# Kernel optimization log

Hardware: AMD Instinct MI355X
Metric: run time of the kernel (lower is better)

Reference implementation:

```python
import jax, jax.numpy as jnp
import numpy as np

N = 100000   # nodes
E = 1200000  # edges
IN, HID, OUT = 64, 64, 64
G = 64       # graphs in the batch


def setup_inputs() -> dict:
    key = jax.random.key(0)
    ks = jax.random.split(key, 7)
    x = jax.random.normal(ks[0], (N, IN), dtype=jnp.float32)
    edge_index = jax.random.randint(ks[1], (2, E), 0, N, dtype=jnp.int32)
    batch = jnp.sort(jax.random.randint(ks[2], (N,), 0, G, dtype=jnp.int32))
    W1 = jax.random.normal(ks[3], (IN, HID), dtype=jnp.float32) * (1.0 / np.sqrt(IN))
    b1 = jnp.zeros((HID,), dtype=jnp.float32)
    W2 = jax.random.normal(ks[4], (HID, OUT), dtype=jnp.float32) * (1.0 / np.sqrt(HID))
    b2 = jnp.zeros((OUT,), dtype=jnp.float32)
    return {"x": x, "edge_index": edge_index, "batch": batch,
            "W1": W1, "b1": b1, "W2": W2, "b2": b2}


def _gcn_conv(x, W, b, src, dst, dinv):
    # x' = D^{-1/2} (A + I) D^{-1/2} (x W) + b   (PyG GCNConv with self-loops)
    h = x @ W                                   # [N, F_out]
    norm = dinv[src] * dinv[dst]                # [E]
    agg = jax.ops.segment_sum(h[src] * norm[:, None], dst, num_segments=N)
    agg = agg + h * (dinv * dinv)[:, None]      # self-loop contribution
    return agg + b


def reference(x, edge_index, batch, W1, b1, W2, b2):
    src, dst = edge_index[0], edge_index[1]
    # degree with self-loops, counted at the aggregation target (PyG convention)
    deg = jax.ops.segment_sum(jnp.ones((E,), x.dtype), dst, num_segments=N) + 1.0
    dinv = jax.lax.rsqrt(deg)

    h1 = jax.nn.relu(_gcn_conv(x, W1, b1, src, dst, dinv))   # [N, HID]
    s1 = jax.ops.segment_sum(h1, batch, num_segments=G)      # [G, HID]
    h2 = jax.nn.relu(_gcn_conv(h1, W2, b2, src, dst, dinv))  # [N, OUT]
    s2 = jax.ops.segment_sum(h2, batch, num_segments=G)      # [G, OUT]
    return h2, jnp.concatenate([s1, s2], axis=1)
```

## Files before the change

kernel.cpp:

```cpp
#include <hip/hip_runtime.h>


#define FDIM 64
#define BSHIFT 7
#define MAXNB 1024
#define BCAP 4096

__device__ __forceinline__ unsigned short f2bf(float f) {
    union { float f; unsigned int u; } a; a.f = f;
    unsigned int u = a.u;
    unsigned int r = u + 0x7fffu + ((u >> 16) & 1u);
    return (unsigned short)(r >> 16);
}
__device__ __forceinline__ float bf2f(unsigned short s) {
    union { unsigned int u; float f; } a; a.u = ((unsigned int)s) << 16;
    return a.f;
}

__global__ __launch_bounds__(256) void k_hist(const int* __restrict__ dst, int E, int NB,
                                              int* __restrict__ bucketCnt,
                                              const int* __restrict__ batch, int N, int G,
                                              int* __restrict__ gstart) {
    if (blockIdx.x >= 256) {
        int i = (blockIdx.x - 256) * 256 + threadIdx.x;
        if (i >= N) return;
        int b = batch[i];
        if (i == 0) { for (int g = 0; g <= b; g++) gstart[g] = 0; }
        else {
            int p = batch[i - 1];
            for (int g = p + 1; g <= b; g++) gstart[g] = i;
        }
        if (i == N - 1) { for (int g = b + 1; g <= G; g++) gstart[g] = N; }
        return;
    }
    __shared__ int h[MAXNB];
    for (int i = threadIdx.x; i < NB; i += 256) h[i] = 0;
    __syncthreads();
    for (int e = blockIdx.x * blockDim.x + threadIdx.x; e < E; e += 256 * 256)
        atomicAdd(&h[dst[e] >> BSHIFT], 1);
    __syncthreads();
    for (int i = threadIdx.x; i < NB; i += 256) {
        int c = h[i];
        if (c) atomicAdd(&bucketCnt[i], c);
    }
}

__global__ __launch_bounds__(256) void k_bscat(const int* __restrict__ src,
                                               const int* __restrict__ dst, int E, int NB,
                                               const int* __restrict__ bucketCnt,
                                               int* __restrict__ bucketFill,
                                               unsigned int* __restrict__ ebuf) {
    __shared__ int hist[MAXNB];
    __shared__ int base[MAXNB];
    __shared__ int sc[256];
    int t = threadIdx.x;
    for (int i = t; i < MAXNB; i += 256) hist[i] = 0;
    __syncthreads();
    int e0 = blockIdx.x * 4096;
    int s[16], d[16], r[16];
#pragma unroll
    for (int k = 0; k < 16; k++) {
        int e = e0 + k * 256 + t;
        bool valid = e < E;
        s[k] = valid ? src[e] : 0;
        d[k] = valid ? dst[e] : 0;
        r[k] = valid ? atomicAdd(&hist[d[k] >> BSHIFT], 1) : 0;
    }
    int c0 = bucketCnt[t * 4 + 0], c1 = bucketCnt[t * 4 + 1];
    int c2 = bucketCnt[t * 4 + 2], c3 = bucketCnt[t * 4 + 3];
    int ssum = c0 + c1 + c2 + c3;
    sc[t] = ssum;
    __syncthreads();
    for (int off = 1; off < 256; off <<= 1) {
        int u = (t >= off) ? sc[t - off] : 0;
        __syncthreads();
        sc[t] += u;
        __syncthreads();
    }
    int run = sc[t] - ssum;
    base[t * 4 + 0] = run; run += c0;
    base[t * 4 + 1] = run; run += c1;
    base[t * 4 + 2] = run; run += c2;
    base[t * 4 + 3] = run;
    __syncthreads();
    for (int i = t; i < NB; i += 256) {
        int c = hist[i];
        if (c) base[i] += atomicAdd(&bucketFill[i], c);
    }
    __syncthreads();
#pragma unroll
    for (int k = 0; k < 16; k++) {
        int e = e0 + k * 256 + t;
        if (e < E)
            ebuf[base[d[k] >> BSHIFT] + r[k]] =
                (unsigned int)s[k] | ((unsigned int)(d[k] & 127) << 17);
    }
}

__global__ __launch_bounds__(256) void k_bsort(const unsigned int* __restrict__ ebuf,
                                               const int* __restrict__ bucketCnt, int N,
                                               int* __restrict__ row_ptr,
                                               int* __restrict__ row_blocks,
                                               int* __restrict__ col,
                                               float* __restrict__ dinv) {
    __shared__ int cntL[128];
    __shared__ int scanL[128];
    __shared__ int fillL[128];
    __shared__ int colL[BCAP];
    __shared__ int padT;
    __shared__ int red[4];
    int b = blockIdx.x;
    int n0 = b << BSHIFT;
    int nCnt = N - n0; if (nCnt > 128) nCnt = 128;
    int t = threadIdx.x;
    int part = 0;
    for (int i = t; i < b; i += 256) part += bucketCnt[i];
    for (int off = 32; off; off >>= 1) part += __shfl_down(part, off);
    if ((t & 63) == 0) red[t >> 6] = part;
    __syncthreads();
    int lo = red[0] + red[1] + red[2] + red[3];
    int hi = lo + bucketCnt[b];
    int outBase = ((lo + 7) & ~7) + (b << 10);
    if (t < 128) { cntL[t] = 0; fillL[t] = 0; }
    __syncthreads();
    for (int e = lo + t; e < hi; e += 256)
        atomicAdd(&cntL[ebuf[e] >> 17], 1);
    __syncthreads();
    int pc = 0;
    if (t < 128) { pc = (cntL[t] + 7) & ~7; scanL[t] = pc; }
    __syncthreads();
    for (int off = 1; off < 128; off <<= 1) {
        int u = (t >= off && t < 128) ? scanL[t - off] : 0;
        __syncthreads();
        if (t < 128) scanL[t] += u;
        __syncthreads();
    }
    if (t == 127) padT = scanL[127];
    if (t < nCnt) {
        int ex = scanL[t] - pc;
        row_ptr[n0 + t] = outBase + ex;
        row_blocks[n0 + t] = pc >> 3;
        dinv[n0 + t] = rsqrtf((float)cntL[t] + 1.0f);
        scanL[t] = ex;
    }
    __syncthreads();
    int padTotal = padT;
    if (padTotal <= BCAP) {
        for (int i = t; i < padTotal; i += 256) colL[i] = N;
        __syncthreads();
        for (int e = lo + t; e < hi; e += 256) {
            unsigned int pr = ebuf[e];
            int d = pr >> 17;
            int r = scanL[d] + atomicAdd(&fillL[d], 1);
            colL[r] = (int)(pr & 0x1FFFFu);
        }
        __syncthreads();
        for (int i = t; i < padTotal; i += 256) col[outBase + i] = colL[i];
    } else {
        for (int e = lo + t; e < hi; e += 256) {
            unsigned int pr = ebuf[e];
            int d = pr >> 17;
            int r = scanL[d] + atomicAdd(&fillL[d], 1);
            col[outBase + r] = (int)(pr & 0x1FFFFu);
        }
        __syncthreads();
        if (t < nCnt) {
            int pcl = (cntL[t] + 7) & ~7;
            for (int i = cntL[t]; i < pcl; i++) col[outBase + scanL[t] + i] = N;
        }
    }
}

__global__ __launch_bounds__(256, 4) void k_gemm_scale(const float* __restrict__ X,
                                                       const float* __restrict__ W,
                                                       const float* __restrict__ dinv, int N,
                                                       unsigned short* __restrict__ Gb) {
    __shared__ float4 Ws[64 * 16];
    __shared__ float Xs[64][68];
    int tid = threadIdx.x;
    ushort4* GB4 = (ushort4*)Gb;
    if (blockIdx.x == 0 && tid < 16) {
        ushort4 z; z.x = z.y = z.z = z.w = 0;
        GB4[(size_t)N * 16 + tid] = z;
    }
    const float4* W4 = (const float4*)W;
    for (int i = tid; i < 64 * 16; i += 256) Ws[i] = W4[i];
    int rowBase = blockIdx.x * 64;
    for (int i = tid; i < 1024; i += 256) {
        int r = i >> 4, f4 = i & 15;
        float4 v = make_float4(0.f, 0.f, 0.f, 0.f);
        if (rowBase + r < N) v = ((const float4*)X)[(size_t)(rowBase + r) * 16 + f4];
        *(float4*)&Xs[r][f4 * 4] = v;
    }
    __syncthreads();
    int r0 = (tid >> 4) * 4;
    int c4 = tid & 15;
    float4 acc0 = make_float4(0,0,0,0), acc1 = acc0, acc2 = acc0, acc3 = acc0;
#pragma unroll 16
    for (int k = 0; k < 64; k++) {
        float4 w = Ws[k * 16 + c4];
        float x0 = Xs[r0 + 0][k], x1 = Xs[r0 + 1][k], x2 = Xs[r0 + 2][k], x3 = Xs[r0 + 3][k];
        acc0.x += x0 * w.x; acc0.y += x0 * w.y; acc0.z += x0 * w.z; acc0.w += x0 * w.w;
        acc1.x += x1 * w.x; acc1.y += x1 * w.y; acc1.z += x1 * w.z; acc1.w += x1 * w.w;
        acc2.x += x2 * w.x; acc2.y += x2 * w.y; acc2.z += x2 * w.z; acc2.w += x2 * w.w;
        acc3.x += x3 * w.x; acc3.y += x3 * w.y; acc3.z += x3 * w.z; acc3.w += x3 * w.w;
    }
    float4 a[4] = {acc0, acc1, acc2, acc3};
#pragma unroll
    for (int i = 0; i < 4; i++) {
        int row = rowBase + r0 + i;
        if (row < N) {
            float dn = dinv[row];
            ushort4 pk;
            pk.x = f2bf(a[i].x * dn);
            pk.y = f2bf(a[i].y * dn);
            pk.z = f2bf(a[i].z * dn);
            pk.w = f2bf(a[i].w * dn);
            GB4[(size_t)row * 16 + c4] = pk;
        }
    }
}

__global__ __launch_bounds__(256) void k_agg(const unsigned short* __restrict__ Gb,
                                             const int* __restrict__ row_ptr,
                                             const int* __restrict__ row_blocks,
                                             const int* __restrict__ col,
                                             const float* __restrict__ dinv,
                                             const float* __restrict__ bias, int N,
                                             float* __restrict__ Out) {
    int w = threadIdx.x >> 6;
    int c = threadIdx.x & 63;
    int n = blockIdx.x * 4 + w;
    if (n >= N) return;
    int e = row_ptr[n];
    int nb8 = row_blocks[n];
    float acc = bf2f(Gb[(size_t)n * FDIM + c]);
    for (; nb8 >= 2; nb8 -= 2, e += 16) {
        int4 ca = *(const int4*)(col + e);
        int4 cb = *(const int4*)(col + e + 4);
        int4 cc = *(const int4*)(col + e + 8);
        int4 cd = *(const int4*)(col + e + 12);
        int s0  = __builtin_amdgcn_readfirstlane(ca.x);
        int s1  = __builtin_amdgcn_readfirstlane(ca.y);
        int s2  = __builtin_amdgcn_readfirstlane(ca.z);
        int s3  = __builtin_amdgcn_readfirstlane(ca.w);
        int s4  = __builtin_amdgcn_readfirstlane(cb.x);
        int s5  = __builtin_amdgcn_readfirstlane(cb.y);
        int s6  = __builtin_amdgcn_readfirstlane(cb.z);
        int s7  = __builtin_amdgcn_readfirstlane(cb.w);
        int s8  = __builtin_amdgcn_readfirstlane(cc.x);
        int s9  = __builtin_amdgcn_readfirstlane(cc.y);
        int s10 = __builtin_amdgcn_readfirstlane(cc.z);
        int s11 = __builtin_amdgcn_readfirstlane(cc.w);
        int s12 = __builtin_amdgcn_readfirstlane(cd.x);
        int s13 = __builtin_amdgcn_readfirstlane(cd.y);
        int s14 = __builtin_amdgcn_readfirstlane(cd.z);
        int s15 = __builtin_amdgcn_readfirstlane(cd.w);
        float a0  = bf2f(Gb[(size_t)s0  * FDIM + c]);
        float a1  = bf2f(Gb[(size_t)s1  * FDIM + c]);
        float a2  = bf2f(Gb[(size_t)s2  * FDIM + c]);
        float a3  = bf2f(Gb[(size_t)s3  * FDIM + c]);
        float a4  = bf2f(Gb[(size_t)s4  * FDIM + c]);
        float a5  = bf2f(Gb[(size_t)s5  * FDIM + c]);
        float a6  = bf2f(Gb[(size_t)s6  * FDIM + c]);
        float a7  = bf2f(Gb[(size_t)s7  * FDIM + c]);
        float a8  = bf2f(Gb[(size_t)s8  * FDIM + c]);
        float a9  = bf2f(Gb[(size_t)s9  * FDIM + c]);
        float a10 = bf2f(Gb[(size_t)s10 * FDIM + c]);
        float a11 = bf2f(Gb[(size_t)s11 * FDIM + c]);
        float a12 = bf2f(Gb[(size_t)s12 * FDIM + c]);
        float a13 = bf2f(Gb[(size_t)s13 * FDIM + c]);
        float a14 = bf2f(Gb[(size_t)s14 * FDIM + c]);
        float a15 = bf2f(Gb[(size_t)s15 * FDIM + c]);
        acc += (((a0 + a1) + (a2 + a3)) + ((a4 + a5) + (a6 + a7)))
             + (((a8 + a9) + (a10 + a11)) + ((a12 + a13) + (a14 + a15)));
    }
    if (nb8) {
        int4 ca = *(const int4*)(col + e);
        int4 cb = *(const int4*)(col + e + 4);
        int s0 = __builtin_amdgcn_readfirstlane(ca.x);
        int s1 = __builtin_amdgcn_readfirstlane(ca.y);
        int s2 = __builtin_amdgcn_readfirstlane(ca.z);
        int s3 = __builtin_amdgcn_readfirstlane(ca.w);
        int s4 = __builtin_amdgcn_readfirstlane(cb.x);
        int s5 = __builtin_amdgcn_readfirstlane(cb.y);
        int s6 = __builtin_amdgcn_readfirstlane(cb.z);
        int s7 = __builtin_amdgcn_readfirstlane(cb.w);
        float a0 = bf2f(Gb[(size_t)s0 * FDIM + c]);
        float a1 = bf2f(Gb[(size_t)s1 * FDIM + c]);
        float a2 = bf2f(Gb[(size_t)s2 * FDIM + c]);
        float a3 = bf2f(Gb[(size_t)s3 * FDIM + c]);
        float a4 = bf2f(Gb[(size_t)s4 * FDIM + c]);
        float a5 = bf2f(Gb[(size_t)s5 * FDIM + c]);
        float a6 = bf2f(Gb[(size_t)s6 * FDIM + c]);
        float a7 = bf2f(Gb[(size_t)s7 * FDIM + c]);
        acc += ((a0 + a1) + (a2 + a3)) + ((a4 + a5) + (a6 + a7));
    }
    float v = fmaxf(acc * dinv[n] + bias[c], 0.f);
    Out[(size_t)n * FDIM + c] = v;
}

__global__ __launch_bounds__(256) void k_pool(const float4* __restrict__ H1,
                                              const float4* __restrict__ H2,
                                              const int* __restrict__ gstart,
                                              float* __restrict__ pool) {
    int g = blockIdx.x & 63;
    int layer = blockIdx.x >> 6;
    const float4* H = layer ? H2 : H1;
    int colOff = layer ? 64 : 0;
    int lo = gstart[g], hi = gstart[g + 1];
    int c4 = threadIdx.x & 15;
    int rl = threadIdx.x >> 4;
    float4 acc = make_float4(0.f, 0.f, 0.f, 0.f);
    for (int r = lo + rl; r < hi; r += 16) {
        float4 v = H[(size_t)r * 16 + c4];
        acc.x += v.x; acc.y += v.y; acc.z += v.z; acc.w += v.w;
    }
    __shared__ float4 sm[16][16];
    sm[rl][c4] = acc;
    __syncthreads();
    if (rl == 0) {
        float4 s = sm[0][c4];
#pragma unroll
        for (int k = 1; k < 16; k++) {
            float4 v = sm[k][c4];
            s.x += v.x; s.y += v.y; s.z += v.z; s.w += v.w;
        }
        float* dst = &pool[(size_t)g * 128 + colOff + c4 * 4];
        dst[0] = s.x; dst[1] = s.y; dst[2] = s.z; dst[3] = s.w;
    }
}

static inline size_t align256(size_t x) { return (x + 255) & ~(size_t)255; }

extern "C" void kernel_launch(void* const* d_in, const int* in_sizes, int n_in,
                              void* d_out, int out_size, void* d_ws, size_t ws_size,
                              hipStream_t stream) {
    const float* x     = (const float*)d_in[0];
    const int*   ei    = (const int*)d_in[1];
    const int*   batch = (const int*)d_in[2];
    const float* W1    = (const float*)d_in[3];
    const float* b1    = (const float*)d_in[4];
    const float* W2    = (const float*)d_in[5];
    const float* b2    = (const float*)d_in[6];

    const int N = in_sizes[0] / FDIM;
    const int E = in_sizes[1] / 2;
    const int G = 64;
    const int NB = (N + 127) >> BSHIFT;
    const int* src = ei;
    const int* dst = ei + E;

    char* p = (char*)d_ws;
    int* row_ptr     = (int*)p; p += align256(((size_t)N + 1) * 4);
    int* row_blocks  = (int*)p; p += align256((size_t)N * 4);
    int* col         = (int*)p; p += align256(((size_t)E + (size_t)(NB + 1) * 1024) * 4);
    int* bucketCnt   = (int*)p; p += align256((size_t)2 * MAXNB * 4);
    int* bucketFill  = bucketCnt + MAXNB;
    int* gstart      = (int*)p; p += align256((size_t)(G + 1) * 4);
    float* dinv      = (float*)p; p += align256((size_t)N * 4);
    float* g         = (float*)p; p += align256(((size_t)N + 1) * FDIM * 4);
    float* h1        = (float*)p; p += align256((size_t)N * FDIM * 4);
    unsigned int* ebuf = (unsigned int*)g;
    unsigned short* gb = (unsigned short*)g;

    float* out  = (float*)d_out;
    float* h2   = out;
    float* pool = out + (size_t)N * FDIM;

    hipMemsetAsync(bucketCnt, 0, (size_t)2 * MAXNB * 4, stream);

    int nb = (N + 255) / 256;
    int gemmB = (N + 63) / 64;
    int aggB  = (N + 3) / 4;
    int scatB = (E + 4095) / 4096;

    k_hist<<<256 + nb, 256, 0, stream>>>(dst, E, NB, bucketCnt, batch, N, G, gstart);
    k_bscat<<<scatB, 256, 0, stream>>>(src, dst, E, NB, bucketCnt, bucketFill, ebuf);
    k_bsort<<<NB, 256, 0, stream>>>(ebuf, bucketCnt, N, row_ptr, row_blocks, col, dinv);

    k_gemm_scale<<<gemmB, 256, 0, stream>>>(x, W1, dinv, N, gb);
    k_agg<<<aggB, 256, 0, stream>>>(gb, row_ptr, row_blocks, col, dinv, b1, N, h1);

    k_gemm_scale<<<gemmB, 256, 0, stream>>>(h1, W2, dinv, N, gb);
    k_agg<<<aggB, 256, 0, stream>>>(gb, row_ptr, row_blocks, col, dinv, b2, N, h2);

    k_pool<<<2 * G, 256, 0, stream>>>((const float4*)h1, (const float4*)h2, gstart, pool);
}
```

Baseline: 262.0 us.

## Fuse first GEMM into preprocessing and second GEMM into layer-1 aggregation

The first X·W1 GEMM now runs inside the histogram/gstart preprocessing launch. It no longer depends on dinv, because the source-side normalisation moved into the gather loop as per-neighbour dinv loads. The second GEMM is fused into the layer-1 aggregation epilogue, with W2 held in shared memory, and h1 is stored as bf16 for pooling, which removes two launches and the fp32 h1 round-trip. The cost is extra scattered dinv loads per edge, a per-node 64x64 matvec through LDS in the aggregation kernel, and bf16 rounding of h1 in the pooled sums.

```diff
diff --git a/kernel.cpp b/kernel.cpp
--- a/kernel.cpp
+++ b/kernel.cpp
@@ -17,36 +17,83 @@
     return a.f;
 }
 
-__global__ __launch_bounds__(256) void k_hist(const int* __restrict__ dst, int E, int NB,
-                                              int* __restrict__ bucketCnt,
-                                              const int* __restrict__ batch, int N, int G,
-                                              int* __restrict__ gstart) {
-    if (blockIdx.x >= 256) {
-        int i = (blockIdx.x - 256) * 256 + threadIdx.x;
-        if (i >= N) return;
-        int b = batch[i];
-        if (i == 0) { for (int g = 0; g <= b; g++) gstart[g] = 0; }
-        else {
-            int p = batch[i - 1];
-            for (int g = p + 1; g <= b; g++) gstart[g] = i;
-        }
-        if (i == N - 1) { for (int g = b + 1; g <= G; g++) gstart[g] = N; }
+__global__ __launch_bounds__(256, 4) void k_pre(
+    const int* __restrict__ dstp, int E, int NB,
+    const int* __restrict__ batch, int N, int G, int nbB,
+    const float* __restrict__ x, const float* __restrict__ W1,
+    int* __restrict__ bucketCnt, int* __restrict__ gstart,
+    unsigned short* __restrict__ gb1) {
+    __shared__ __align__(16) char sm[33792];
+    int tid = threadIdx.x;
+    int bx = blockIdx.x;
+    if (bx < 256) {
+        int* h = (int*)sm;
+        for (int i = tid; i < NB; i += 256) h[i] = 0;
+        __syncthreads();
+        for (int e = bx * 256 + tid; e < E; e += 256 * 256)
+            atomicAdd(&h[dstp[e] >> BSHIFT], 1);
+        __syncthreads();
+        for (int i = tid; i < NB; i += 256) {
+            int c = h[i];
+            if (c) atomicAdd(&bucketCnt[i], c);
+        }
         return;
     }
-    __shared__ int h[MAXNB];
-    for (int i = threadIdx.x; i < NB; i += 256) h[i] = 0;
-    __syncthreads();
-    for (int e = blockIdx.x * blockDim.x + threadIdx.x; e < E; e += 256 * 256)
-        atomicAdd(&h[dst[e] >> BSHIFT], 1);
-    __syncthreads();
-    for (int i = threadIdx.x; i < NB; i += 256) {
-        int c = h[i];
-        if (c) atomicAdd(&bucketCnt[i], c);
+    if (bx < 256 + nbB) {
+        int i = (bx - 256) * 256 + tid;
+        if (i < N) {
+            int b = batch[i];
+            if (i == 0) { for (int g = 0; g <= b; g++) gstart[g] = 0; }
+            else {
+                int pp = batch[i - 1];
+                for (int g = pp + 1; g <= b; g++) gstart[g] = i;
+            }
+            if (i == N - 1) { for (int g = b + 1; g <= G; g++) gstart[g] = N; }
+        }
+        return;
+    }
+    int vb = bx - 256 - nbB;
+    float4* Ws = (float4*)sm;
+    float (*Xs)[68] = (float(*)[68])(sm + 16384);
+    ushort4* GB4 = (ushort4*)gb1;
+    if (vb == 0 && tid < 16) GB4[(size_t)N * 16 + tid] = make_ushort4(0, 0, 0, 0);
+    const float4* W4 = (const float4*)W1;
+    for (int i = tid; i < 1024; i += 256) Ws[i] = W4[i];
+    int rowBase = vb * 64;
+    for (int i = tid; i < 1024; i += 256) {
+        int r = i >> 4, f4 = i & 15;
+        float4 v = make_float4(0.f, 0.f, 0.f, 0.f);
+        if (rowBase + r < N) v = ((const float4*)x)[(size_t)(rowBase + r) * 16 + f4];
+        *(float4*)&Xs[r][f4 * 4] = v;
+    }
+    __syncthreads();
+    int r0 = (tid >> 4) * 4;
+    int c4 = tid & 15;
+    float4 acc0 = make_float4(0,0,0,0), acc1 = acc0, acc2 = acc0, acc3 = acc0;
+#pragma unroll 16
+    for (int k = 0; k < 64; k++) {
+        float4 w = Ws[k * 16 + c4];
+        float x0 = Xs[r0 + 0][k], x1 = Xs[r0 + 1][k], x2 = Xs[r0 + 2][k], x3 = Xs[r0 + 3][k];
+        acc0.x += x0 * w.x; acc0.y += x0 * w.y; acc0.z += x0 * w.z; acc0.w += x0 * w.w;
+        acc1.x += x1 * w.x; acc1.y += x1 * w.y; acc1.z += x1 * w.z; acc1.w += x1 * w.w;
+        acc2.x += x2 * w.x; acc2.y += x2 * w.y; acc2.z += x2 * w.z; acc2.w += x2 * w.w;
+        acc3.x += x3 * w.x; acc3.y += x3 * w.y; acc3.z += x3 * w.z; acc3.w += x3 * w.w;
+    }
+    float4 a[4] = {acc0, acc1, acc2, acc3};
+#pragma unroll
+    for (int i = 0; i < 4; i++) {
+        int row = rowBase + r0 + i;
+        if (row < N) {
+            ushort4 pk;
+            pk.x = f2bf(a[i].x); pk.y = f2bf(a[i].y);
+            pk.z = f2bf(a[i].z); pk.w = f2bf(a[i].w);
+            GB4[(size_t)row * 16 + c4] = pk;
+        }
     }
 }
 
 __global__ __launch_bounds__(256) void k_bscat(const int* __restrict__ src,
-                                               const int* __restrict__ dst, int E, int NB,
+                                               const int* __restrict__ dstp, int E, int NB,
                                                const int* __restrict__ bucketCnt,
                                                int* __restrict__ bucketFill,
                                                unsigned int* __restrict__ ebuf) {
@@ -63,7 +110,7 @@
         int e = e0 + k * 256 + t;
         bool valid = e < E;
         s[k] = valid ? src[e] : 0;
-        d[k] = valid ? dst[e] : 0;
+        d[k] = valid ? dstp[e] : 0;
         r[k] = valid ? atomicAdd(&hist[d[k] >> BSHIFT], 1) : 0;
     }
     int c0 = bucketCnt[t * 4 + 0], c1 = bucketCnt[t * 4 + 1];
@@ -113,6 +160,7 @@
     int n0 = b << BSHIFT;
     int nCnt = N - n0; if (nCnt > 128) nCnt = 128;
     int t = threadIdx.x;
+    if (b == 0 && t == 0) dinv[N] = 0.f;
     int part = 0;
     for (int i = t; i < b; i += 256) part += bucketCnt[i];
     for (int off = 32; off; off >>= 1) part += __shfl_down(part, off);
@@ -171,70 +219,26 @@
     }
 }
 
-__global__ __launch_bounds__(256, 4) void k_gemm_scale(const float* __restrict__ X,
-                                                       const float* __restrict__ W,
-                                                       const float* __restrict__ dinv, int N,
-                                                       unsigned short* __restrict__ Gb) {
-    __shared__ float4 Ws[64 * 16];
-    __shared__ float Xs[64][68];
+__global__ __launch_bounds__(256) void k_agg1(
+    const unsigned short* __restrict__ Gb1,
+    const int* __restrict__ row_ptr, const int* __restrict__ row_blocks,
+    const int* __restrict__ col, const float* __restrict__ dinv,
+    const float* __restrict__ b1, const float* __restrict__ W2, int N,
+    unsigned short* __restrict__ H1b, unsigned short* __restrict__ Gb2) {
+    __shared__ float W2s[64][65];
+    __shared__ float hrow[4][64];
     int tid = threadIdx.x;
-    ushort4* GB4 = (ushort4*)Gb;
-    if (blockIdx.x == 0 && tid < 16) {
-        ushort4 z; z.x = z.y = z.z = z.w = 0;
-        GB4[(size_t)N * 16 + tid] = z;
-    }
-    const float4* W4 = (const float4*)W;
-    for (int i = tid; i < 64 * 16; i += 256) Ws[i] = W4[i];
-    int rowBase = blockIdx.x * 64;
-    for (int i = tid; i < 1024; i += 256) {
-        int r = i >> 4, f4 = i & 15;
-        float4 v = make_float4(0.f, 0.f, 0.f, 0.f);
-        if (rowBase + r < N) v = ((const float4*)X)[(size_t)(rowBase + r) * 16 + f4];
-        *(float4*)&Xs[r][f4 * 4] = v;
-    }
-    __syncthreads();
-    int r0 = (tid >> 4) * 4;
-    int c4 = tid & 15;
-    float4 acc0 = make_float4(0,0,0,0), acc1 = acc0, acc2 = acc0, acc3 = acc0;
-#pragma unroll 16
-    for (int k = 0; k < 64; k++) {
-        float4 w = Ws[k * 16 + c4];
-        float x0 = Xs[r0 + 0][k], x1 = Xs[r0 + 1][k], x2 = Xs[r0 + 2][k], x3 = Xs[r0 + 3][k];
-        acc0.x += x0 * w.x; acc0.y += x0 * w.y; acc0.z += x0 * w.z; acc0.w += x0 * w.w;
-        acc1.x += x1 * w.x; acc1.y += x1 * w.y; acc1.z += x1 * w.z; acc1.w += x1 * w.w;
-        acc2.x += x2 * w.x; acc2.y += x2 * w.y; acc2.z += x2 * w.z; acc2.w += x2 * w.w;
-        acc3.x += x3 * w.x; acc3.y += x3 * w.y; acc3.z += x3 * w.z; acc3.w += x3 * w.w;
-    }
-    float4 a[4] = {acc0, acc1, acc2, acc3};
-#pragma unroll
-    for (int i = 0; i < 4; i++) {
-        int row = rowBase + r0 + i;
-        if (row < N) {
-            float dn = dinv[row];
-            ushort4 pk;
-            pk.x = f2bf(a[i].x * dn);
-            pk.y = f2bf(a[i].y * dn);
-            pk.z = f2bf(a[i].z * dn);
-            pk.w = f2bf(a[i].w * dn);
-            GB4[(size_t)row * 16 + c4] = pk;
-        }
-    }
-}
-
-__global__ __launch_bounds__(256) void k_agg(const unsigned short* __restrict__ Gb,
-                                             const int* __restrict__ row_ptr,
-                                             const int* __restrict__ row_blocks,
-                                             const int* __restrict__ col,
-                                             const float* __restrict__ dinv,
-                                             const float* __restrict__ bias, int N,
-                                             float* __restrict__ Out) {
-    int w = threadIdx.x >> 6;
-    int c = threadIdx.x & 63;
+    if (blockIdx.x == 0 && tid < 16)
+        ((ushort4*)Gb2)[(size_t)N * 16 + tid] = make_ushort4(0, 0, 0, 0);
+    for (int i = tid; i < 4096; i += 256) W2s[i >> 6][i & 63] = W2[i];
+    __syncthreads();
+    int w = tid >> 6, c = tid & 63;
     int n = blockIdx.x * 4 + w;
     if (n >= N) return;
     int e = row_ptr[n];
     int nb8 = row_blocks[n];
-    float acc = bf2f(Gb[(size_t)n * FDIM + c]);
+    float dn = dinv[n];
+    float acc = dn * bf2f(Gb1[(size_t)n * FDIM + c]);
     for (; nb8 >= 2; nb8 -= 2, e += 16) {
         int4 ca = *(const int4*)(col + e);
         int4 cb = *(const int4*)(col + e + 4);
@@ -256,24 +260,28 @@
         int s13 = __builtin_amdgcn_readfirstlane(cd.y);
         int s14 = __builtin_amdgcn_readfirstlane(cd.z);
         int s15 = __builtin_amdgcn_readfirstlane(cd.w);
-        float a0  = bf2f(Gb[(size_t)s0  * FDIM + c]);
-        float a1  = bf2f(Gb[(size_t)s1  * FDIM + c]);
-        float a2  = bf2f(Gb[(size_t)s2  * FDIM + c]);
-        float a3  = bf2f(Gb[(size_t)s3  * FDIM + c]);
-        float a4  = bf2f(Gb[(size_t)s4  * FDIM + c]);
-        float a5  = bf2f(Gb[(size_t)s5  * FDIM + c]);
-        float a6  = bf2f(Gb[(size_t)s6  * FDIM + c]);
-        float a7  = bf2f(Gb[(size_t)s7  * FDIM + c]);
-        float a8  = bf2f(Gb[(size_t)s8  * FDIM + c]);
-        float a9  = bf2f(Gb[(size_t)s9  * FDIM + c]);
-        float a10 = bf2f(Gb[(size_t)s10 * FDIM + c]);
-        float a11 = bf2f(Gb[(size_t)s11 * FDIM + c]);
-        float a12 = bf2f(Gb[(size_t)s12 * FDIM + c]);
-        float a13 = bf2f(Gb[(size_t)s13 * FDIM + c]);
-        float a14 = bf2f(Gb[(size_t)s14 * FDIM + c]);
-        float a15 = bf2f(Gb[(size_t)s15 * FDIM + c]);
-        acc += (((a0 + a1) + (a2 + a3)) + ((a4 + a5) + (a6 + a7)))
-             + (((a8 + a9) + (a10 + a11)) + ((a12 + a13) + (a14 + a15)));
+        float d0 = dinv[s0],  d1 = dinv[s1],  d2 = dinv[s2],  d3 = dinv[s3];
+        float d4 = dinv[s4],  d5 = dinv[s5],  d6 = dinv[s6],  d7 = dinv[s7];
+        float d8 = dinv[s8],  d9 = dinv[s9],  d10 = dinv[s10], d11 = dinv[s11];
+        float d12 = dinv[s12], d13 = dinv[s13], d14 = dinv[s14], d15 = dinv[s15];
+        float a0  = bf2f(Gb1[(size_t)s0  * FDIM + c]);
+        float a1  = bf2f(Gb1[(size_t)s1  * FDIM + c]);
+        float a2  = bf2f(Gb1[(size_t)s2  * FDIM + c]);
+        float a3  = bf2f(Gb1[(size_t)s3  * FDIM + c]);
+        float a4  = bf2f(Gb1[(size_t)s4  * FDIM + c]);
+        float a5  = bf2f(Gb1[(size_t)s5  * FDIM + c]);
+        float a6  = bf2f(Gb1[(size_t)s6  * FDIM + c]);
+        float a7  = bf2f(Gb1[(size_t)s7  * FDIM + c]);
+        float a8  = bf2f(Gb1[(size_t)s8  * FDIM + c]);
+        float a9  = bf2f(Gb1[(size_t)s9  * FDIM + c]);
+        float a10 = bf2f(Gb1[(size_t)s10 * FDIM + c]);
+        float a11 = bf2f(Gb1[(size_t)s11 * FDIM + c]);
+        float a12 = bf2f(Gb1[(size_t)s12 * FDIM + c]);
+        float a13 = bf2f(Gb1[(size_t)s13 * FDIM + c]);
+        float a14 = bf2f(Gb1[(size_t)s14 * FDIM + c]);
+        float a15 = bf2f(Gb1[(size_t)s15 * FDIM + c]);
+        acc += ((d0*a0 + d1*a1) + (d2*a2 + d3*a3)) + ((d4*a4 + d5*a5) + (d6*a6 + d7*a7))
+             + ((d8*a8 + d9*a9) + (d10*a10 + d11*a11)) + ((d12*a12 + d13*a13) + (d14*a14 + d15*a15));
     }
     if (nb8) {
         int4 ca = *(const int4*)(col + e);
@@ -286,35 +294,133 @@
         int s5 = __builtin_amdgcn_readfirstlane(cb.y);
         int s6 = __builtin_amdgcn_readfirstlane(cb.z);
         int s7 = __builtin_amdgcn_readfirstlane(cb.w);
-        float a0 = bf2f(Gb[(size_t)s0 * FDIM + c]);
-        float a1 = bf2f(Gb[(size_t)s1 * FDIM + c]);
-        float a2 = bf2f(Gb[(size_t)s2 * FDIM + c]);
-        float a3 = bf2f(Gb[(size_t)s3 * FDIM + c]);
-        float a4 = bf2f(Gb[(size_t)s4 * FDIM + c]);
-        float a5 = bf2f(Gb[(size_t)s5 * FDIM + c]);
-        float a6 = bf2f(Gb[(size_t)s6 * FDIM + c]);
-        float a7 = bf2f(Gb[(size_t)s7 * FDIM + c]);
-        acc += ((a0 + a1) + (a2 + a3)) + ((a4 + a5) + (a6 + a7));
-    }
-    float v = fmaxf(acc * dinv[n] + bias[c], 0.f);
-    Out[(size_t)n * FDIM + c] = v;
-}
-
-__global__ __launch_bounds__(256) void k_pool(const float4* __restrict__ H1,
+        float d0 = dinv[s0], d1 = dinv[s1], d2 = dinv[s2], d3 = dinv[s3];
+        float d4 = dinv[s4], d5 = dinv[s5], d6 = dinv[s6], d7 = dinv[s7];
+        float a0 = bf2f(Gb1[(size_t)s0 * FDIM + c]);
+        float a1 = bf2f(Gb1[(size_t)s1 * FDIM + c]);
+        float a2 = bf2f(Gb1[(size_t)s2 * FDIM + c]);
+        float a3 = bf2f(Gb1[(size_t)s3 * FDIM + c]);
+        float a4 = bf2f(Gb1[(size_t)s4 * FDIM + c]);
+        float a5 = bf2f(Gb1[(size_t)s5 * FDIM + c]);
+        float a6 = bf2f(Gb1[(size_t)s6 * FDIM + c]);
+        float a7 = bf2f(Gb1[(size_t)s7 * FDIM + c]);
+        acc += ((d0*a0 + d1*a1) + (d2*a2 + d3*a3)) + ((d4*a4 + d5*a5) + (d6*a6 + d7*a7));
+    }
+    float v = fmaxf(acc * dn + b1[c], 0.f);
+    H1b[(size_t)n * FDIM + c] = f2bf(v);
+    hrow[w][c] = v;
+    float acc2 = 0.f;
+#pragma unroll 8
+    for (int k = 0; k < 64; k++)
+        acc2 += hrow[w][k] * W2s[k][c];
+    Gb2[(size_t)n * FDIM + c] = f2bf(acc2);
+}
+
+__global__ __launch_bounds__(256) void k_agg2(
+    const unsigned short* __restrict__ Gb2,
+    const int* __restrict__ row_ptr, const int* __restrict__ row_blocks,
+    const int* __restrict__ col, const float* __restrict__ dinv,
+    const float* __restrict__ b2, int N, float* __restrict__ Out) {
+    int tid = threadIdx.x;
+    int w = tid >> 6, c = tid & 63;
+    int n = blockIdx.x * 4 + w;
+    if (n >= N) return;
+    int e = row_ptr[n];
+    int nb8 = row_blocks[n];
+    float dn = dinv[n];
+    float acc = dn * bf2f(Gb2[(size_t)n * FDIM + c]);
+    for (; nb8 >= 2; nb8 -= 2, e += 16) {
+        int4 ca = *(const int4*)(col + e);
+        int4 cb = *(const int4*)(col + e + 4);
+        int4 cc = *(const int4*)(col + e + 8);
+        int4 cd = *(const int4*)(col + e + 12);
+        int s0  = __builtin_amdgcn_readfirstlane(ca.x);
+        int s1  = __builtin_amdgcn_readfirstlane(ca.y);
+        int s2  = __builtin_amdgcn_readfirstlane(ca.z);
+        int s3  = __builtin_amdgcn_readfirstlane(ca.w);
+        int s4  = __builtin_amdgcn_readfirstlane(cb.x);
+        int s5  = __builtin_amdgcn_readfirstlane(cb.y);
+        int s6  = __builtin_amdgcn_readfirstlane(cb.z);
+        int s7  = __builtin_amdgcn_readfirstlane(cb.w);
+        int s8  = __builtin_amdgcn_readfirstlane(cc.x);
+        int s9  = __builtin_amdgcn_readfirstlane(cc.y);
+        int s10 = __builtin_amdgcn_readfirstlane(cc.z);
+        int s11 = __builtin_amdgcn_readfirstlane(cc.w);
+        int s12 = __builtin_amdgcn_readfirstlane(cd.x);
+        int s13 = __builtin_amdgcn_readfirstlane(cd.y);
+        int s14 = __builtin_amdgcn_readfirstlane(cd.z);
+        int s15 = __builtin_amdgcn_readfirstlane(cd.w);
+        float d0 = dinv[s0],  d1 = dinv[s1],  d2 = dinv[s2],  d3 = dinv[s3];
+        float d4 = dinv[s4],  d5 = dinv[s5],  d6 = dinv[s6],  d7 = dinv[s7];
+        float d8 = dinv[s8],  d9 = dinv[s9],  d10 = dinv[s10], d11 = dinv[s11];
+        float d12 = dinv[s12], d13 = dinv[s13], d14 = dinv[s14], d15 = dinv[s15];
+        float a0  = bf2f(Gb2[(size_t)s0  * FDIM + c]);
+        float a1  = bf2f(Gb2[(size_t)s1  * FDIM + c]);
+        float a2  = bf2f(Gb2[(size_t)s2  * FDIM + c]);
+        float a3  = bf2f(Gb2[(size_t)s3  * FDIM + c]);
+        float a4  = bf2f(Gb2[(size_t)s4  * FDIM + c]);
+        float a5  = bf2f(Gb2[(size_t)s5  * FDIM + c]);
+        float a6  = bf2f(Gb2[(size_t)s6  * FDIM + c]);
+        float a7  = bf2f(Gb2[(size_t)s7  * FDIM + c]);
+        float a8  = bf2f(Gb2[(size_t)s8  * FDIM + c]);
+        float a9  = bf2f(Gb2[(size_t)s9  * FDIM + c]);
+        float a10 = bf2f(Gb2[(size_t)s10 * FDIM + c]);
+        float a11 = bf2f(Gb2[(size_t)s11 * FDIM + c]);
+        float a12 = bf2f(Gb2[(size_t)s12 * FDIM + c]);
+        float a13 = bf2f(Gb2[(size_t)s13 * FDIM + c]);
+        float a14 = bf2f(Gb2[(size_t)s14 * FDIM + c]);
+        float a15 = bf2f(Gb2[(size_t)s15 * FDIM + c]);
+        acc += ((d0*a0 + d1*a1) + (d2*a2 + d3*a3)) + ((d4*a4 + d5*a5) + (d6*a6 + d7*a7))
+             + ((d8*a8 + d9*a9) + (d10*a10 + d11*a11)) + ((d12*a12 + d13*a13) + (d14*a14 + d15*a15));
+    }
+    if (nb8) {
+        int4 ca = *(const int4*)(col + e);
+        int4 cb = *(const int4*)(col + e + 4);
+        int s0 = __builtin_amdgcn_readfirstlane(ca.x);
+        int s1 = __builtin_amdgcn_readfirstlane(ca.y);
+        int s2 = __builtin_amdgcn_readfirstlane(ca.z);
+        int s3 = __builtin_amdgcn_readfirstlane(ca.w);
+        int s4 = __builtin_amdgcn_readfirstlane(cb.x);
+        int s5 = __builtin_amdgcn_readfirstlane(cb.y);
+        int s6 = __builtin_amdgcn_readfirstlane(cb.z);
+        int s7 = __builtin_amdgcn_readfirstlane(cb.w);
+        float d0 = dinv[s0], d1 = dinv[s1], d2 = dinv[s2], d3 = dinv[s3];
+        float d4 = dinv[s4], d5 = dinv[s5], d6 = dinv[s6], d7 = dinv[s7];
+        float a0 = bf2f(Gb2[(size_t)s0 * FDIM + c]);
+        float a1 = bf2f(Gb2[(size_t)s1 * FDIM + c]);
+        float a2 = bf2f(Gb2[(size_t)s2 * FDIM + c]);
+        float a3 = bf2f(Gb2[(size_t)s3 * FDIM + c]);
+        float a4 = bf2f(Gb2[(size_t)s4 * FDIM + c]);
+        float a5 = bf2f(Gb2[(size_t)s5 * FDIM + c]);
+        float a6 = bf2f(Gb2[(size_t)s6 * FDIM + c]);
+        float a7 = bf2f(Gb2[(size_t)s7 * FDIM + c]);
+        acc += ((d0*a0 + d1*a1) + (d2*a2 + d3*a3)) + ((d4*a4 + d5*a5) + (d6*a6 + d7*a7));
+    }
+    Out[(size_t)n * FDIM + c] = fmaxf(acc * dn + b2[c], 0.f);
+}
+
+__global__ __launch_bounds__(256) void k_pool(const unsigned short* __restrict__ H1b,
                                               const float4* __restrict__ H2,
                                               const int* __restrict__ gstart,
                                               float* __restrict__ pool) {
     int g = blockIdx.x & 63;
     int layer = blockIdx.x >> 6;
-    const float4* H = layer ? H2 : H1;
-    int colOff = layer ? 64 : 0;
     int lo = gstart[g], hi = gstart[g + 1];
     int c4 = threadIdx.x & 15;
     int rl = threadIdx.x >> 4;
     float4 acc = make_float4(0.f, 0.f, 0.f, 0.f);
-    for (int r = lo + rl; r < hi; r += 16) {
-        float4 v = H[(size_t)r * 16 + c4];
-        acc.x += v.x; acc.y += v.y; acc.z += v.z; acc.w += v.w;
+    if (layer == 0) {
+        const ushort4* H = (const ushort4*)H1b;
+        for (int r = lo + rl; r < hi; r += 16) {
+            ushort4 u = H[(size_t)r * 16 + c4];
+            acc.x += bf2f(u.x); acc.y += bf2f(u.y);
+            acc.z += bf2f(u.z); acc.w += bf2f(u.w);
+        }
+    } else {
+        for (int r = lo + rl; r < hi; r += 16) {
+            float4 v = H2[(size_t)r * 16 + c4];
+            acc.x += v.x; acc.y += v.y; acc.z += v.z; acc.w += v.w;
+        }
     }
     __shared__ float4 sm[16][16];
     sm[rl][c4] = acc;
@@ -326,8 +432,8 @@
             float4 v = sm[k][c4];
             s.x += v.x; s.y += v.y; s.z += v.z; s.w += v.w;
         }
-        float* dst = &pool[(size_t)g * 128 + colOff + c4 * 4];
-        dst[0] = s.x; dst[1] = s.y; dst[2] = s.z; dst[3] = s.w;
+        float* dstq = &pool[(size_t)g * 128 + layer * 64 + c4 * 4];
+        dstq[0] = s.x; dstq[1] = s.y; dstq[2] = s.z; dstq[3] = s.w;
     }
 }
 
@@ -358,11 +464,11 @@
     int* bucketCnt   = (int*)p; p += align256((size_t)2 * MAXNB * 4);
     int* bucketFill  = bucketCnt + MAXNB;
     int* gstart      = (int*)p; p += align256((size_t)(G + 1) * 4);
-    float* dinv      = (float*)p; p += align256((size_t)N * 4);
-    float* g         = (float*)p; p += align256(((size_t)N + 1) * FDIM * 4);
-    float* h1        = (float*)p; p += align256((size_t)N * FDIM * 4);
-    unsigned int* ebuf = (unsigned int*)g;
-    unsigned short* gb = (unsigned short*)g;
+    float* dinv      = (float*)p; p += align256(((size_t)N + 1) * 4);
+    unsigned short* gb1 = (unsigned short*)p; p += align256(((size_t)N + 1) * FDIM * 2);
+    unsigned short* gb2 = (unsigned short*)p; p += align256(((size_t)N + 1) * FDIM * 2);
+    unsigned short* h1b = (unsigned short*)p; p += align256((size_t)N * FDIM * 2);
+    unsigned int* ebuf = (unsigned int*)h1b;
 
     float* out  = (float*)d_out;
     float* h2   = out;
@@ -370,20 +476,17 @@
 
     hipMemsetAsync(bucketCnt, 0, (size_t)2 * MAXNB * 4, stream);
 
-    int nb = (N + 255) / 256;
+    int nbB   = (N + 255) / 256;
     int gemmB = (N + 63) / 64;
     int aggB  = (N + 3) / 4;
     int scatB = (E + 4095) / 4096;
 
-    k_hist<<<256 + nb, 256, 0, stream>>>(dst, E, NB, bucketCnt, batch, N, G, gstart);
+    k_pre<<<256 + nbB + gemmB, 256, 0, stream>>>(dst, E, NB, batch, N, G, nbB,
+                                                 x, W1, bucketCnt, gstart, gb1);
     k_bscat<<<scatB, 256, 0, stream>>>(src, dst, E, NB, bucketCnt, bucketFill, ebuf);
     k_bsort<<<NB, 256, 0, stream>>>(ebuf, bucketCnt, N, row_ptr, row_blocks, col, dinv);
-
-    k_gemm_scale<<<gemmB, 256, 0, stream>>>(x, W1, dinv, N, gb);
-    k_agg<<<aggB, 256, 0, stream>>>(gb, row_ptr, row_blocks, col, dinv, b1, N, h1);
-
-    k_gemm_scale<<<gemmB, 256, 0, stream>>>(h1, W2, dinv, N, gb);
-    k_agg<<<aggB, 256, 0, stream>>>(gb, row_ptr, row_blocks, col, dinv, b2, N, h2);
-
-    k_pool<<<2 * G, 256, 0, stream>>>((const float4*)h1, (const float4*)h2, gstart, pool);
-}
+    k_agg1<<<aggB, 256, 0, stream>>>(gb1, row_ptr, row_blocks, col, dinv, b1, W2, N,
+                                     h1b, gb2);
+    k_agg2<<<aggB, 256, 0, stream>>>(gb2, row_ptr, row_blocks, col, dinv, b2, N, h2);
+    k_pool<<<2 * G, 256, 0, stream>>>(h1b, (const float4*)h2, gstart, pool);
+}
```

Result: slower. 287.2 us (+9.6%).
